# Optimization experiments

Hardware: AMD Instinct MI355X
Metric: run time of the kernel (lower is better)

Reference implementation:

```python
import jax, jax.numpy as jnp
import numpy as np

NODE_DIM = 64
DEPTH = 2
N = 50000          # node_size
DEG = 24           # average degree
E = N * DEG        # triple_size = 1.2M edges
R = 500            # rel_size
FEAT = NODE_DIM * (DEPTH + 1)  # 192


def _l2norm(x, eps=1e-12):
    # torch F.normalize(p=2): x / max(||x||, eps)
    n = jnp.sqrt(jnp.sum(x * x, axis=-1, keepdims=True))
    return x / jnp.maximum(n, eps)


def setup_inputs() -> dict:
    key = jax.random.key(0)
    ks = jax.random.split(key, 8)
    features = jax.random.normal(ks[0], (N, NODE_DIM), jnp.float32)
    rel_emb = jax.random.normal(ks[1], (R, NODE_DIM), jnp.float32)
    # duplicate-free edge list, rows sorted (matches a coalesced sparse adj)
    rows = jnp.repeat(jnp.arange(N, dtype=jnp.int32), DEG)
    offs = jnp.tile(1 + jnp.arange(DEG, dtype=jnp.int32) * 7, N)
    cols = (rows + offs) % N
    adj = jnp.stack([rows, cols])  # [2, E]
    # sparse [E, R] triple->relation matrix: one relation per triple
    r_index = jnp.stack([jnp.arange(E, dtype=jnp.int32),
                         jax.random.randint(ks[2], (E,), 0, R, jnp.int32)])
    r_val = jax.random.uniform(ks[3], (E,), jnp.float32, 0.5, 1.5)
    # params (xavier-ish scales)
    proxy = jax.random.normal(ks[4], (64, FEAT), jnp.float32) * (1.0 / np.sqrt(FEAT))
    gate_w = jax.random.normal(ks[5], (FEAT, FEAT), jnp.float32) * (1.0 / np.sqrt(FEAT))
    gate_b = jnp.zeros((FEAT,), jnp.float32)
    attn_kernels = jax.random.normal(ks[6], (DEPTH, NODE_DIM), jnp.float32) * 0.1
    return {"features": features, "rel_emb": rel_emb, "proxy": proxy,
            "gate_w": gate_w, "gate_b": gate_b, "attn_kernels": attn_kernels,
            "adj": adj, "r_index": r_index, "r_val": r_val,
            "triple_size": E, "rel_size": R, "node_size": N}


def reference(features, rel_emb, proxy, gate_w, gate_b, attn_kernels,
              adj, r_index, r_val, triple_size, rel_size, node_size):
    feats = jnp.tanh(features)
    outs = [feats]
    dst = adj[0]  # rows: softmax / scatter-sum segment ids
    src = adj[1]  # cols: neighbor gather ids
    for l in range(attn_kernels.shape[0]):
        neighs = feats[src]                                  # [E, d] gather
        # sparse.mm(tri_rel, rel_emb): sum_k r_val * rel_emb[rel_id] per triple
        tri_rel = jax.ops.segment_sum(r_val[:, None] * rel_emb[r_index[1]],
                                      r_index[0], num_segments=triple_size)
        tri_rel = _l2norm(tri_rel)                           # [E, d]
        # relational reflection: h - 2 <h, r> r
        neighs = neighs - 2.0 * jnp.sum(neighs * tri_rel, axis=1, keepdims=True) * tri_rel
        att = jnp.einsum('ed,d->e', tri_rel, attn_kernels[l])  # [E]
        # sparse softmax over rows of adjacency (segment softmax over dst)
        m = jax.ops.segment_max(att, dst, num_segments=node_size)
        ex = jnp.exp(att - m[dst])
        denom = jax.ops.segment_sum(ex, dst, num_segments=node_size)
        w = ex / denom[dst]
        new_f = jax.ops.segment_sum(neighs * w[:, None], dst, num_segments=node_size)
        feats = jnp.tanh(new_f)
        outs.append(feats)
    outputs = jnp.concatenate(outs, axis=-1)                 # [N, feat]
    proxy_att = jax.nn.softmax(_l2norm(outputs) @ _l2norm(proxy).T, axis=-1)
    proxy_feature = outputs - proxy_att @ proxy
    gate = jax.nn.sigmoid(proxy_feature @ gate_w.T + gate_b)
    return gate * outputs + (1.0 - gate) * proxy_feature
```

## Files before the change

### kernel.cpp

```cpp
#include <hip/hip_runtime.h>
#include <hip/hip_bf16.h>
#include <cstdint>
#include <cstddef>

#define N_NODES 50000
#define DEG     24
#define NEDGE   (N_NODES*DEG)
#define RSZ     500
#define NDIM    64
#define FEATD   192

#define LSTR    200

#define LGRID   1568
#define LCHUNK  196

typedef short bf16x8 __attribute__((ext_vector_type(8)));
typedef float f32x4  __attribute__((ext_vector_type(4)));

__device__ __forceinline__ unsigned short f2bf(float f) {
    unsigned u = __builtin_bit_cast(unsigned, f);
    unsigned r = (u + 0x7fffu + ((u >> 16) & 1u)) >> 16;
    return (unsigned short)r;
}
__device__ __forceinline__ float bf2f(unsigned short s) {
    unsigned u = ((unsigned)s) << 16;
    return __builtin_bit_cast(float, u);
}
__device__ __forceinline__ float fast_tanh(float x) {
    float e = __expf(2.f * x);
    return 1.f - 2.f / (e + 1.f);
}

__global__ __launch_bounds__(256) void k_prep(const float* __restrict__ features,
                                              const float* __restrict__ rel_emb,
                                              const float* __restrict__ attn_k,
                                              const float* __restrict__ proxy,
                                              const float* __restrict__ gate_w,
                                              const int* __restrict__ src,
                                              const int* __restrict__ rel,
                                              float* __restrict__ outputs,
                                              float* __restrict__ fin0,
                                              float* __restrict__ reln,
                                              float* __restrict__ expdot,
                                              float* __restrict__ pninv,
                                              unsigned short* __restrict__ B1,
                                              unsigned short* __restrict__ B2,
                                              unsigned short* __restrict__ B3,
                                              unsigned int* __restrict__ pedge) {
    int b = blockIdx.x;
    if (b < 3125) {
        int t = b * 256 + threadIdx.x;
        int idx4 = t * 4;
        int row = idx4 >> 6, col = idx4 & 63;
        float4 f = *reinterpret_cast<const float4*>(features + idx4);
        float4 o;
        o.x = fast_tanh(f.x); o.y = fast_tanh(f.y);
        o.z = fast_tanh(f.z); o.w = fast_tanh(f.w);
        *reinterpret_cast<float4*>(outputs + (size_t)row * FEATD + col) = o;
        *reinterpret_cast<float4*>(fin0 + idx4) = o;
    } else if (b < 3250) {
        int lane = threadIdx.x & 63;
        int row = (b - 3125) * 4 + (threadIdx.x >> 6);
        float v = rel_emb[row * 64 + lane];
        float ss = v * v;
        for (int m = 1; m < 64; m <<= 1) ss += __shfl_xor(ss, m);
        float inv = 1.f / fmaxf(sqrtf(ss), 1e-12f);
        float rn = v * inv;
        reln[row * 64 + lane] = rn;
        float d0 = rn * attn_k[lane];
        float d1 = rn * attn_k[64 + lane];
        for (int m = 1; m < 64; m <<= 1) { d0 += __shfl_xor(d0, m); d1 += __shfl_xor(d1, m); }
        if (lane == 0) { expdot[row] = __expf(d0); expdot[RSZ + row] = __expf(d1); }
    } else if (b < 3266) {
        int lane = threadIdx.x & 63;
        int row = (b - 3250) * 4 + (threadIdx.x >> 6);
        const float* p = proxy + (size_t)row * FEATD;
        float a = p[lane], bb = p[64 + lane], c = p[128 + lane];
        float ss = a * a + bb * bb + c * c;
        for (int m = 1; m < 64; m <<= 1) ss += __shfl_xor(ss, m);
        if (lane == 0) pninv[row] = 1.f / fmaxf(sqrtf(ss), 1e-12f);
    } else if (b < 3506) {
        int idx = (b - 3266) * 256 + threadIdx.x;
        int j = idx & 7, lane = (idx >> 3) & 63;
        int t = idx >> 9;
        int lane16 = lane & 15, quad = lane >> 4;
        if (t < 24) {
            int kt = t >> 2, nt = t & 3;
            int k = kt * 32 + quad * 8 + j, n = nt * 16 + lane16;
            B1[idx] = f2bf(proxy[(size_t)n * FEATD + k]);
        } else if (t < 48) {
            int tt = t - 24, kt = tt / 12, nt = tt % 12;
            int k = kt * 32 + quad * 8 + j, n = nt * 16 + lane16;
            B2[idx - 12288] = f2bf(proxy[(size_t)k * FEATD + n]);
        } else {
            int tt = t - 48, kt = tt / 12, nt = tt % 12;
            int k = kt * 32 + quad * 8 + j, n = nt * 16 + lane16;
            B3[idx - 24576] = f2bf(gate_w[(size_t)n * FEATD + k]);
        }
    } else {
        int t = (b - 3506) * 256 + threadIdx.x;
        if (t < NEDGE / 4) {
            int4 s4 = *reinterpret_cast<const int4*>(src + t * 4);
            int4 r4 = *reinterpret_cast<const int4*>(rel + t * 4);
            uint4 o;
            o.x = (unsigned)s4.x | ((unsigned)r4.x << 16);
            o.y = (unsigned)s4.y | ((unsigned)r4.y << 16);
            o.z = (unsigned)s4.z | ((unsigned)r4.z << 16);
            o.w = (unsigned)s4.w | ((unsigned)r4.w << 16);
            *reinterpret_cast<uint4*>(pedge + t * 4) = o;
        }
    }
}

__global__ __launch_bounds__(256) void k_layer(const unsigned int* __restrict__ pedge,
                                               const float* __restrict__ reln,
                                               const float* __restrict__ expdot_l,
                                               const float* __restrict__ fin,
                                               float* __restrict__ fout,
                                               float* __restrict__ outputs,
                                               int colout) {
    int b = blockIdx.x;
    int lb = (b & 7) * LCHUNK + (b >> 3);
    int lane8 = threadIdx.x & 7;
    int node = lb * 32 + (threadIdx.x >> 3);
    if (node >= N_NODES) return;
    int ebase = node * DEG;
    unsigned pk[DEG];
#pragma unroll
    for (int k = 0; k < DEG; k++) pk[k] = pedge[ebase + k];
    float a0 = 0.f, a1 = 0.f, a2 = 0.f, a3 = 0.f;
    float a4 = 0.f, a5 = 0.f, a6 = 0.f, a7 = 0.f, den = 0.f;
#pragma unroll 4
    for (int k = 0; k < DEG; k++) {
        unsigned p = pk[k];
        int s = p & 0xFFFF;
        int r = p >> 16;
        float ex = expdot_l[r];
        const float* tp = reln + (size_t)r * 64 + lane8 * 8;
        const float* np = fin + (size_t)s * 64 + lane8 * 8;
        float4 t0 = *reinterpret_cast<const float4*>(tp);
        float4 t1v = *reinterpret_cast<const float4*>(tp + 4);
        float4 n0 = *reinterpret_cast<const float4*>(np);
        float4 n1v = *reinterpret_cast<const float4*>(np + 4);
        float pd = t0.x * n0.x + t0.y * n0.y + t0.z * n0.z + t0.w * n0.w
                 + t1v.x * n1v.x + t1v.y * n1v.y + t1v.z * n1v.z + t1v.w * n1v.w;
        pd += __shfl_xor(pd, 1); pd += __shfl_xor(pd, 2); pd += __shfl_xor(pd, 4);
        float t1 = -2.f * pd * ex;
        a0 = fmaf(ex, n0.x, fmaf(t1, t0.x, a0));
        a1 = fmaf(ex, n0.y, fmaf(t1, t0.y, a1));
        a2 = fmaf(ex, n0.z, fmaf(t1, t0.z, a2));
        a3 = fmaf(ex, n0.w, fmaf(t1, t0.w, a3));
        a4 = fmaf(ex, n1v.x, fmaf(t1, t1v.x, a4));
        a5 = fmaf(ex, n1v.y, fmaf(t1, t1v.y, a5));
        a6 = fmaf(ex, n1v.z, fmaf(t1, t1v.z, a6));
        a7 = fmaf(ex, n1v.w, fmaf(t1, t1v.w, a7));
        den += ex;
    }
    float id = 1.f / den;
    float4 o0, o1;
    o0.x = fast_tanh(a0 * id); o0.y = fast_tanh(a1 * id);
    o0.z = fast_tanh(a2 * id); o0.w = fast_tanh(a3 * id);
    o1.x = fast_tanh(a4 * id); o1.y = fast_tanh(a5 * id);
    o1.z = fast_tanh(a6 * id); o1.w = fast_tanh(a7 * id);
    float* orow = outputs + (size_t)node * FEATD + colout + lane8 * 8;
    *reinterpret_cast<float4*>(orow) = o0;
    *reinterpret_cast<float4*>(orow + 4) = o1;
    if (fout) {
        float* f = fout + (size_t)node * 64 + lane8 * 8;
        *reinterpret_cast<float4*>(f) = o0;
        *reinterpret_cast<float4*>(f + 4) = o1;
    }
}

__global__ __launch_bounds__(256) void k_gate(const float* __restrict__ outputs,
                                              const unsigned short* __restrict__ B1,
                                              const unsigned short* __restrict__ B2,
                                              const unsigned short* __restrict__ B3,
                                              const float* __restrict__ pninv,
                                              const float* __restrict__ gate_b,
                                              float* __restrict__ dout) {
    __shared__ unsigned short lds[4][16 * LSTR];
    int wv = threadIdx.x >> 6, lane = threadIdx.x & 63;
    int tile = blockIdx.x * 4 + wv;
    if (tile > N_NODES / 16 - 1) tile = N_NODES / 16 - 1;
    int row0 = tile * 16, lane16 = lane & 15, quad = lane >> 4;
    unsigned short* L = lds[wv];

    const float* arow = outputs + (size_t)(row0 + lane16) * FEATD + quad * 8;
    bf16x8 af[6];
    float ss = 0.f;
#pragma unroll
    for (int kt = 0; kt < 6; kt++) {
        float4 p0 = *reinterpret_cast<const float4*>(arow + kt * 32);
        float4 p1 = *reinterpret_cast<const float4*>(arow + kt * 32 + 4);
        ss += p0.x * p0.x + p0.y * p0.y + p0.z * p0.z + p0.w * p0.w;
        ss += p1.x * p1.x + p1.y * p1.y + p1.z * p1.z + p1.w * p1.w;
        bf16x8 a;
        a[0] = (short)f2bf(p0.x); a[1] = (short)f2bf(p0.y);
        a[2] = (short)f2bf(p0.z); a[3] = (short)f2bf(p0.w);
        a[4] = (short)f2bf(p1.x); a[5] = (short)f2bf(p1.y);
        a[6] = (short)f2bf(p1.z); a[7] = (short)f2bf(p1.w);
        af[kt] = a;
    }
    ss += __shfl_xor(ss, 16); ss += __shfl_xor(ss, 32);
    float inv = 1.f / fmaxf(sqrtf(ss), 1e-12f);
    float pni[4];
#pragma unroll
    for (int nt = 0; nt < 4; nt++) pni[nt] = pninv[nt * 16 + lane16];
    f32x4 acc4[4];
#pragma unroll
    for (int nt = 0; nt < 4; nt++) acc4[nt] = (f32x4){0.f, 0.f, 0.f, 0.f};
#pragma unroll
    for (int kt = 0; kt < 6; kt++) {
#pragma unroll
        for (int nt = 0; nt < 4; nt++) {
            bf16x8 bfr = *reinterpret_cast<const bf16x8*>(B1 + ((size_t)(kt * 4 + nt) * 64 + lane) * 8);
            acc4[nt] = __builtin_amdgcn_mfma_f32_16x16x32_bf16(af[kt], bfr, acc4[nt], 0, 0, 0);
        }
    }
#pragma unroll
    for (int r = 0; r < 4; r++) {
        int rowloc = quad * 4 + r;
        float invr = __shfl(inv, rowloc);
        float v0 = acc4[0][r] * invr * pni[0], v1 = acc4[1][r] * invr * pni[1];
        float v2 = acc4[2][r] * invr * pni[2], v3 = acc4[3][r] * invr * pni[3];
        float m = fmaxf(fmaxf(v0, v1), fmaxf(v2, v3));
        m = fmaxf(m, __shfl_xor(m, 1)); m = fmaxf(m, __shfl_xor(m, 2));
        m = fmaxf(m, __shfl_xor(m, 4)); m = fmaxf(m, __shfl_xor(m, 8));
        float e0 = __expf(v0 - m), e1 = __expf(v1 - m);
        float e2 = __expf(v2 - m), e3 = __expf(v3 - m);
        float s = e0 + e1 + e2 + e3;
        s += __shfl_xor(s, 1); s += __shfl_xor(s, 2);
        s += __shfl_xor(s, 4); s += __shfl_xor(s, 8);
        float rs = 1.f / s;
        L[rowloc * LSTR + lane16]      = f2bf(e0 * rs);
        L[rowloc * LSTR + 16 + lane16] = f2bf(e1 * rs);
        L[rowloc * LSTR + 32 + lane16] = f2bf(e2 * rs);
        L[rowloc * LSTR + 48 + lane16] = f2bf(e3 * rs);
    }
    __syncthreads();

    f32x4 acc[12];
#pragma unroll
    for (int nt = 0; nt < 12; nt++) acc[nt] = (f32x4){0.f, 0.f, 0.f, 0.f};
#pragma unroll
    for (int kt = 0; kt < 2; kt++) {
        bf16x8 a = *reinterpret_cast<const bf16x8*>(L + lane16 * LSTR + kt * 32 + quad * 8);
#pragma unroll
        for (int nt = 0; nt < 12; nt++) {
            bf16x8 bfr = *reinterpret_cast<const bf16x8*>(B2 + ((size_t)(kt * 12 + nt) * 64 + lane) * 8);
            acc[nt] = __builtin_amdgcn_mfma_f32_16x16x32_bf16(a, bfr, acc[nt], 0, 0, 0);
        }
    }
    float oreg[12][4];
#pragma unroll
    for (int nt = 0; nt < 12; nt++) {
#pragma unroll
        for (int r = 0; r < 4; r++) {
            int rowloc = quad * 4 + r;
            size_t idx = (size_t)(row0 + rowloc) * FEATD + nt * 16 + lane16;
            float o = outputs[idx];
            oreg[nt][r] = o;
            L[rowloc * LSTR + nt * 16 + lane16] = f2bf(o - acc[nt][r]);
        }
    }
    __syncthreads();

#pragma unroll
    for (int nt = 0; nt < 12; nt++) acc[nt] = (f32x4){0.f, 0.f, 0.f, 0.f};
#pragma unroll
    for (int kt = 0; kt < 6; kt++) {
        bf16x8 a = *reinterpret_cast<const bf16x8*>(L + lane16 * LSTR + kt * 32 + quad * 8);
#pragma unroll
        for (int nt = 0; nt < 12; nt++) {
            bf16x8 bfr = *reinterpret_cast<const bf16x8*>(B3 + ((size_t)(kt * 12 + nt) * 64 + lane) * 8);
            acc[nt] = __builtin_amdgcn_mfma_f32_16x16x32_bf16(a, bfr, acc[nt], 0, 0, 0);
        }
    }

#pragma unroll
    for (int nt = 0; nt < 12; nt++) {
        float bias = gate_b[nt * 16 + lane16];
#pragma unroll
        for (int r = 0; r < 4; r++) {
            int rowloc = quad * 4 + r;
            size_t idx = (size_t)(row0 + rowloc) * FEATD + nt * 16 + lane16;
            float z = acc[nt][r] + bias;
            float g = 1.f / (1.f + __expf(-z));
            float pf = bf2f(L[rowloc * LSTR + nt * 16 + lane16]);
            dout[idx] = pf + g * (oreg[nt][r] - pf);
        }
    }
}

extern "C" void kernel_launch(void* const* d_in, const int* in_sizes, int n_in,
                              void* d_out, int out_size, void* d_ws, size_t ws_size,
                              hipStream_t stream) {
    (void)in_sizes; (void)n_in; (void)out_size; (void)ws_size;
    const float* features = (const float*)d_in[0];
    const float* rel_emb  = (const float*)d_in[1];
    const float* proxy    = (const float*)d_in[2];
    const float* gate_w   = (const float*)d_in[3];
    const float* gate_b   = (const float*)d_in[4];
    const float* attn_k   = (const float*)d_in[5];
    const int*   adj      = (const int*)d_in[6];
    const int*   r_index  = (const int*)d_in[7];

    float* outputs = (float*)d_ws;
    float* fin0    = outputs + (size_t)N_NODES * FEATD;
    float* fin1    = fin0 + (size_t)N_NODES * 64;
    float* reln    = fin1 + (size_t)N_NODES * 64;
    float* expdot  = reln + RSZ * 64;
    float* pninv   = expdot + 2 * RSZ;
    unsigned short* B1 = (unsigned short*)(pninv + 64);
    unsigned short* B2 = B1 + 12288;
    unsigned short* B3 = B2 + 12288;
    unsigned int* pedge = (unsigned int*)(B3 + 36864);

    const int* src = adj + NEDGE;
    const int* rel = r_index + NEDGE;

    k_prep  <<<dim3(4678), dim3(256), 0, stream>>>(features, rel_emb, attn_k, proxy, gate_w,
                                                   src, rel, outputs, fin0, reln, expdot,
                                                   pninv, B1, B2, B3, pedge);
    k_layer <<<dim3(LGRID), dim3(256), 0, stream>>>(pedge, reln, expdot,       fin0, fin1,    outputs, 64);
    k_layer <<<dim3(LGRID), dim3(256), 0, stream>>>(pedge, reln, expdot + RSZ, fin1, nullptr, outputs, 128);
    k_gate  <<<dim3(782),  dim3(256), 0, stream>>>(outputs, B1, B2, B3, pninv, gate_b, (float*)d_out);
}
```

Measured before the change: 205.2 us.

## Drop concatenated outputs buffer; gate reads per-layer features, skip softmax max

```diff
diff --git a/kernel.cpp b/kernel.cpp
--- a/kernel.cpp
+++ b/kernel.cpp
@@ -39,7 +39,6 @@
                                               const float* __restrict__ gate_w,
                                               const int* __restrict__ src,
                                               const int* __restrict__ rel,
-                                              float* __restrict__ outputs,
                                               float* __restrict__ fin0,
                                               float* __restrict__ reln,
                                               float* __restrict__ expdot,
@@ -52,12 +51,10 @@
     if (b < 3125) {
         int t = b * 256 + threadIdx.x;
         int idx4 = t * 4;
-        int row = idx4 >> 6, col = idx4 & 63;
         float4 f = *reinterpret_cast<const float4*>(features + idx4);
         float4 o;
         o.x = fast_tanh(f.x); o.y = fast_tanh(f.y);
         o.z = fast_tanh(f.z); o.w = fast_tanh(f.w);
-        *reinterpret_cast<float4*>(outputs + (size_t)row * FEATD + col) = o;
         *reinterpret_cast<float4*>(fin0 + idx4) = o;
     } else if (b < 3250) {
         int lane = threadIdx.x & 63;
@@ -117,9 +114,7 @@
                                                const float* __restrict__ reln,
                                                const float* __restrict__ expdot_l,
                                                const float* __restrict__ fin,
-                                               float* __restrict__ fout,
-                                               float* __restrict__ outputs,
-                                               int colout) {
+                                               float* __restrict__ fout) {
     int b = blockIdx.x;
     int lb = (b & 7) * LCHUNK + (b >> 3);
     int lane8 = threadIdx.x & 7;
@@ -163,17 +158,14 @@
     o0.z = fast_tanh(a2 * id); o0.w = fast_tanh(a3 * id);
     o1.x = fast_tanh(a4 * id); o1.y = fast_tanh(a5 * id);
     o1.z = fast_tanh(a6 * id); o1.w = fast_tanh(a7 * id);
-    float* orow = outputs + (size_t)node * FEATD + colout + lane8 * 8;
-    *reinterpret_cast<float4*>(orow) = o0;
-    *reinterpret_cast<float4*>(orow + 4) = o1;
-    if (fout) {
-        float* f = fout + (size_t)node * 64 + lane8 * 8;
-        *reinterpret_cast<float4*>(f) = o0;
-        *reinterpret_cast<float4*>(f + 4) = o1;
-    }
-}
-
-__global__ __launch_bounds__(256) void k_gate(const float* __restrict__ outputs,
+    float* f = fout + (size_t)node * 64 + lane8 * 8;
+    *reinterpret_cast<float4*>(f) = o0;
+    *reinterpret_cast<float4*>(f + 4) = o1;
+}
+
+__global__ __launch_bounds__(256) void k_gate(const float* __restrict__ fin0,
+                                              const float* __restrict__ fin1,
+                                              const float* __restrict__ fin2,
                                               const unsigned short* __restrict__ B1,
                                               const unsigned short* __restrict__ B2,
                                               const unsigned short* __restrict__ B3,
@@ -186,14 +178,25 @@
     if (tile > N_NODES / 16 - 1) tile = N_NODES / 16 - 1;
     int row0 = tile * 16, lane16 = lane & 15, quad = lane >> 4;
     unsigned short* L = lds[wv];
-
-    const float* arow = outputs + (size_t)(row0 + lane16) * FEATD + quad * 8;
+    const float* fsel[3] = {fin0, fin1, fin2};
+
+    float oreg[12][4];
+#pragma unroll
+    for (int nt = 0; nt < 12; nt++) {
+        const float* f = fsel[nt >> 2];
+#pragma unroll
+        for (int r = 0; r < 4; r++)
+            oreg[nt][r] = f[(size_t)(row0 + quad * 4 + r) * 64 + (nt & 3) * 16 + lane16];
+    }
+
     bf16x8 af[6];
     float ss = 0.f;
 #pragma unroll
     for (int kt = 0; kt < 6; kt++) {
-        float4 p0 = *reinterpret_cast<const float4*>(arow + kt * 32);
-        float4 p1 = *reinterpret_cast<const float4*>(arow + kt * 32 + 4);
+        const float* f = fsel[kt >> 1];
+        const float* arow = f + (size_t)(row0 + lane16) * 64 + (kt & 1) * 32 + quad * 8;
+        float4 p0 = *reinterpret_cast<const float4*>(arow);
+        float4 p1 = *reinterpret_cast<const float4*>(arow + 4);
         ss += p0.x * p0.x + p0.y * p0.y + p0.z * p0.z + p0.w * p0.w;
         ss += p1.x * p1.x + p1.y * p1.y + p1.z * p1.z + p1.w * p1.w;
         bf16x8 a;
@@ -223,13 +226,10 @@
     for (int r = 0; r < 4; r++) {
         int rowloc = quad * 4 + r;
         float invr = __shfl(inv, rowloc);
-        float v0 = acc4[0][r] * invr * pni[0], v1 = acc4[1][r] * invr * pni[1];
-        float v2 = acc4[2][r] * invr * pni[2], v3 = acc4[3][r] * invr * pni[3];
-        float m = fmaxf(fmaxf(v0, v1), fmaxf(v2, v3));
-        m = fmaxf(m, __shfl_xor(m, 1)); m = fmaxf(m, __shfl_xor(m, 2));
-        m = fmaxf(m, __shfl_xor(m, 4)); m = fmaxf(m, __shfl_xor(m, 8));
-        float e0 = __expf(v0 - m), e1 = __expf(v1 - m);
-        float e2 = __expf(v2 - m), e3 = __expf(v3 - m);
+        float e0 = __expf(acc4[0][r] * invr * pni[0]);
+        float e1 = __expf(acc4[1][r] * invr * pni[1]);
+        float e2 = __expf(acc4[2][r] * invr * pni[2]);
+        float e3 = __expf(acc4[3][r] * invr * pni[3]);
         float s = e0 + e1 + e2 + e3;
         s += __shfl_xor(s, 1); s += __shfl_xor(s, 2);
         s += __shfl_xor(s, 4); s += __shfl_xor(s, 8);
@@ -239,7 +239,7 @@
         L[rowloc * LSTR + 32 + lane16] = f2bf(e2 * rs);
         L[rowloc * LSTR + 48 + lane16] = f2bf(e3 * rs);
     }
-    __syncthreads();
+    __threadfence_block();
 
     f32x4 acc[12];
 #pragma unroll
@@ -253,19 +253,16 @@
             acc[nt] = __builtin_amdgcn_mfma_f32_16x16x32_bf16(a, bfr, acc[nt], 0, 0, 0);
         }
     }
-    float oreg[12][4];
+    __threadfence_block();
 #pragma unroll
     for (int nt = 0; nt < 12; nt++) {
 #pragma unroll
         for (int r = 0; r < 4; r++) {
             int rowloc = quad * 4 + r;
-            size_t idx = (size_t)(row0 + rowloc) * FEATD + nt * 16 + lane16;
-            float o = outputs[idx];
-            oreg[nt][r] = o;
-            L[rowloc * LSTR + nt * 16 + lane16] = f2bf(o - acc[nt][r]);
-        }
-    }
-    __syncthreads();
+            L[rowloc * LSTR + nt * 16 + lane16] = f2bf(oreg[nt][r] - acc[nt][r]);
+        }
+    }
+    __threadfence_block();
 
 #pragma unroll
     for (int nt = 0; nt < 12; nt++) acc[nt] = (f32x4){0.f, 0.f, 0.f, 0.f};
@@ -307,10 +304,10 @@
     const int*   adj      = (const int*)d_in[6];
     const int*   r_index  = (const int*)d_in[7];
 
-    float* outputs = (float*)d_ws;
-    float* fin0    = outputs + (size_t)N_NODES * FEATD;
+    float* fin0    = (float*)d_ws;
     float* fin1    = fin0 + (size_t)N_NODES * 64;
-    float* reln    = fin1 + (size_t)N_NODES * 64;
+    float* fin2    = fin1 + (size_t)N_NODES * 64;
+    float* reln    = fin2 + (size_t)N_NODES * 64;
     float* expdot  = reln + RSZ * 64;
     float* pninv   = expdot + 2 * RSZ;
     unsigned short* B1 = (unsigned short*)(pninv + 64);
@@ -322,9 +319,10 @@
     const int* rel = r_index + NEDGE;
 
     k_prep  <<<dim3(4678), dim3(256), 0, stream>>>(features, rel_emb, attn_k, proxy, gate_w,
-                                                   src, rel, outputs, fin0, reln, expdot,
+                                                   src, rel, fin0, reln, expdot,
                                                    pninv, B1, B2, B3, pedge);
-    k_layer <<<dim3(LGRID), dim3(256), 0, stream>>>(pedge, reln, expdot,       fin0, fin1,    outputs, 64);
-    k_layer <<<dim3(LGRID), dim3(256), 0, stream>>>(pedge, reln, expdot + RSZ, fin1, nullptr, outputs, 128);
-    k_gate  <<<dim3(782),  dim3(256), 0, stream>>>(outputs, B1, B2, B3, pninv, gate_b, (float*)d_out);
-}
+    k_layer <<<dim3(LGRID), dim3(256), 0, stream>>>(pedge, reln, expdot,       fin0, fin1);
+    k_layer <<<dim3(LGRID), dim3(256), 0, stream>>>(pedge, reln, expdot + RSZ, fin1, fin2);
+    k_gate  <<<dim3(782),  dim3(256), 0, stream>>>(fin0, fin1, fin2, B1, B2, B3, pninv,
+                                                   gate_b, (float*)d_out);
+}
```

Measured after the change: 205.3 us. Within noise of the previous version (+0.1%).
